# Kernel tuning notes

Measured on AMD Instinct MI355X. Metric: run time of the kernel, lower is better.

Reference implementation:

```python
import jax, jax.numpy as jnp
import numpy as np

N_NODES = 100000
N_EDGES = 1600000
GENE_DIM = 256
HID = 128
NUM_CLASSES = 2
BN_EPS = 1e-5


def setup_inputs() -> dict:
    key = jax.random.key(0)
    ks = jax.random.split(key, 24)
    g = lambda k, shape, scale: (jax.random.normal(k, shape, dtype=jnp.float32) * scale)
    inp = {
        "x": g(ks[0], (N_NODES, GENE_DIM), 1.0),
        "edge_index": jax.random.randint(ks[1], (2, N_EDGES), 0, N_NODES, dtype=jnp.int64),
        # GCNConv weights (glorot-ish scale) and biases
        "W1": g(ks[2], (GENE_DIM, HID), 1.0 / np.sqrt(GENE_DIM)), "b1": jnp.zeros((HID,), jnp.float32),
        "W2": g(ks[3], (HID, 2 * HID), 1.0 / np.sqrt(HID)), "b2": jnp.zeros((2 * HID,), jnp.float32),
        "W3": g(ks[4], (2 * HID, HID), 1.0 / np.sqrt(2 * HID)), "b3": jnp.zeros((HID,), jnp.float32),
        "W4": g(ks[5], (HID, HID // 2), 1.0 / np.sqrt(HID)), "b4": jnp.zeros((HID // 2,), jnp.float32),
        "Wc": g(ks[6], (HID // 2, NUM_CLASSES), 1.0 / np.sqrt(HID // 2)), "bc": jnp.zeros((NUM_CLASSES,), jnp.float32),
        # BatchNorm affine params
        "g1": jnp.ones((HID,), jnp.float32), "be1": jnp.zeros((HID,), jnp.float32),
        "g2": jnp.ones((2 * HID,), jnp.float32), "be2": jnp.zeros((2 * HID,), jnp.float32),
        "g3": jnp.ones((HID,), jnp.float32), "be3": jnp.zeros((HID,), jnp.float32),
        "g4": jnp.ones((HID // 2,), jnp.float32), "be4": jnp.zeros((HID // 2,), jnp.float32),
    }
    return inp


def _batchnorm(h, gamma, beta):
    # training-mode BatchNorm1d: per-feature batch stats (biased variance)
    mean = h.mean(axis=0)
    var = ((h - mean) ** 2).mean(axis=0)
    return gamma * (h - mean) * jax.lax.rsqrt(var + BN_EPS) + beta


def _gcn_conv(h, W, b, src, dst, norm, n):
    # PyG GCNConv: linear transform, then sym-normalized aggregation over
    # edges (self-loops already included in src/dst/norm), then bias.
    m = h @ W                                   # [n, d_out]
    msg = m[src] * norm[:, None]                # [E+n, d_out] gather
    agg = jax.ops.segment_sum(msg, dst, num_segments=n)  # scatter-add
    return agg + b


def reference(x, edge_index, W1, b1, W2, b2, W3, b3, W4, b4, Wc, bc,
              g1, be1, g2, be2, g3, be3, g4, be4):
    n = x.shape[0]
    loop = jnp.arange(n, dtype=edge_index.dtype)
    src = jnp.concatenate([edge_index[0], loop])  # add self-loops
    dst = jnp.concatenate([edge_index[1], loop])
    deg = jax.ops.segment_sum(jnp.ones_like(dst, dtype=x.dtype), dst, num_segments=n)
    dinv = jax.lax.rsqrt(jnp.maximum(deg, 1.0))
    norm = dinv[src] * dinv[dst]                  # D^-1/2 (A+I) D^-1/2

    h = jax.nn.relu(_gcn_conv(x, W1, b1, src, dst, norm, n))
    h = _batchnorm(h, g1, be1)
    h = jax.nn.relu(_gcn_conv(h, W2, b2, src, dst, norm, n))
    h = _batchnorm(h, g2, be2)
    h = jax.nn.relu(_gcn_conv(h, W3, b3, src, dst, norm, n))
    h = _batchnorm(h, g3, be3)
    out4 = jax.nn.relu(_gcn_conv(h, W4, b4, src, dst, norm, n))
    bn4 = _batchnorm(out4, g4, be4)
    logits = bn4 @ Wc + bc
    return (logits, out4, bn4)
```

## Files before the change

### kernel.cpp

```cpp
#include <hip/hip_runtime.h>
#include <hip/hip_bf16.h>

#define N_NODES 100000
#define N_EDGES 1600000
#define NB ((N_NODES + 255) / 256)
#define CHUNK 16384
#define NBLK ((N_EDGES + CHUNK - 1) / CHUNK)

typedef short sh8 __attribute__((ext_vector_type(8)));
typedef float f32x4 __attribute__((ext_vector_type(4)));

__device__ __forceinline__ float bf2f(unsigned short s) {
    return __uint_as_float(((unsigned int)s) << 16);
}
__device__ __forceinline__ unsigned short f2bf(float f) {
    unsigned int u = __float_as_uint(f);
    unsigned int r = (u + 0x7FFFu + ((u >> 16) & 1u)) >> 16;
    return (unsigned short)r;
}
__device__ __forceinline__ float blo(unsigned int u) { return __uint_as_float(u << 16); }
__device__ __forceinline__ float bhi(unsigned int u) { return __uint_as_float(u & 0xffff0000u); }


__global__ __launch_bounds__(256) void k_hist(const int* __restrict__ ei, int* __restrict__ histG) {
    __shared__ int hist[NB];
    int blk = blockIdx.x, t = threadIdx.x;
    for (int b = t; b < NB; b += 256) hist[b] = 0;
    __syncthreads();
    int e0 = blk * CHUNK;
    int e1 = min(e0 + CHUNK, N_EDGES);
    for (int e = e0 + t; e < e1; e += 256) atomicAdd(&hist[ei[N_EDGES + e] >> 8], 1);
    __syncthreads();
    for (int b = t; b < NB; b += 256) histG[b * NBLK + blk] = hist[b];
}

__global__ __launch_bounds__(128) void k_scanrow(int* __restrict__ histG, int* __restrict__ rowsum) {
    __shared__ int sm[128];
    int b = blockIdx.x, t = threadIdx.x;
    int v = (t < NBLK) ? histG[b * NBLK + t] : 0;
    sm[t] = v; __syncthreads();
    for (int d = 1; d < 128; d <<= 1) {
        int add = (t >= d) ? sm[t - d] : 0;
        __syncthreads(); sm[t] += add; __syncthreads();
    }
    if (t < NBLK) histG[b * NBLK + t] = sm[t] - v;
    if (t == 127) rowsum[b] = sm[127];
}

__global__ __launch_bounds__(512) void k_scanbkt(const int* __restrict__ rowsum, int* __restrict__ rowbase) {
    __shared__ int sm[512];
    int t = threadIdx.x;
    int v = (t < NB) ? rowsum[t] : 0;
    sm[t] = v; __syncthreads();
    for (int d = 1; d < 512; d <<= 1) {
        int add = (t >= d) ? sm[t - d] : 0;
        __syncthreads(); sm[t] += add; __syncthreads();
    }
    if (t <= NB) rowbase[t] = sm[t] - v;
}

__global__ __launch_bounds__(256) void k_part(const int* __restrict__ ei, const int* __restrict__ histG,
                                              const int* __restrict__ rowbase, unsigned* __restrict__ pairs) {
    __shared__ int cur[NB];
    int blk = blockIdx.x, t = threadIdx.x;
    for (int b = t; b < NB; b += 256) cur[b] = rowbase[b] + histG[b * NBLK + blk];
    __syncthreads();
    int e0 = blk * CHUNK;
    int e1 = min(e0 + CHUNK, N_EDGES);
    for (int e = e0 + t; e < e1; e += 256) {
        int s = ei[e], d = ei[N_EDGES + e];
        int pos = atomicAdd(&cur[d >> 8], 1);
        pairs[pos] = ((unsigned)s << 8) | (unsigned)(d & 255);
    }
}

__global__ __launch_bounds__(256) void k_bsort(const unsigned* __restrict__ pairs, const int* __restrict__ rowbase,
                                               int* __restrict__ col, int* __restrict__ basep,
                                               int* __restrict__ deg, float* __restrict__ dinv,
                                               float* __restrict__ sdeg) {
    __shared__ int cnt[256];
    __shared__ int sm[256];
    __shared__ int cur[256];
    int b = blockIdx.x, t = threadIdx.x;
    int base = rowbase[b], end = rowbase[b + 1];
    cnt[t] = 0; __syncthreads();
    for (int e = base + t; e < end; e += 256) atomicAdd(&cnt[pairs[e] & 255], 1);
    __syncthreads();
    int v = cnt[t];
    sm[t] = v; __syncthreads();
    for (int d = 1; d < 256; d <<= 1) {
        int add = (t >= d) ? sm[t - d] : 0;
        __syncthreads(); sm[t] += add; __syncthreads();
    }
    int excl = sm[t] - v;
    cur[t] = excl;
    int gd = (b << 8) + t;
    if (gd < N_NODES) {
        basep[gd] = base + excl;
        deg[gd] = v;
        dinv[gd] = rsqrtf((float)(v + 1));
        sdeg[gd] = sqrtf((float)(v + 1));
    }
    __syncthreads();
    for (int e = base + t; e < end; e += 256) {
        unsigned p = pairs[e];
        int pos = atomicAdd(&cur[p & 255], 1);
        col[base + pos] = (int)(p >> 8);
    }
}

__global__ __launch_bounds__(256) void k_svec(const int* __restrict__ col, const int* __restrict__ basep,
                                              const int* __restrict__ deg, const float* __restrict__ dinv,
                                              float* __restrict__ svec) {
    int w = (blockIdx.x * 256 + threadIdx.x) >> 6;
    if (w >= N_NODES) return;
    int lane = threadIdx.x & 63;
    int start = basep[w], cnt = deg[w];
    float s = 0.f;
    for (int j = lane; j < cnt; j += 64) s += dinv[col[start + j]];
#pragma unroll
    for (int off = 32; off; off >>= 1) s += __shfl_down(s, off, 64);
    if (lane == 0) { float di = dinv[w]; svec[w] = di * (s + di); }
}


__global__ void k_wconv_all(const float* __restrict__ W1, const float* __restrict__ W2,
                            const float* __restrict__ W3, const float* __restrict__ W4,
                            unsigned short* __restrict__ Wt1, unsigned short* __restrict__ Wt2,
                            unsigned short* __restrict__ Wt3, unsigned short* __restrict__ Wt4) {
    int idx = blockIdx.x * 256 + threadIdx.x;
    const float* W; unsigned short* Wt; int K, N, base;
    if (idx < 32768)       { W = W1; Wt = Wt1; K = 256; N = 128; base = 0; }
    else if (idx < 65536)  { W = W2; Wt = Wt2; K = 128; N = 256; base = 32768; }
    else if (idx < 98304)  { W = W3; Wt = Wt3; K = 256; N = 128; base = 65536; }
    else if (idx < 106496) { W = W4; Wt = Wt4; K = 128; N = 64;  base = 98304; }
    else return;
    int li = idx - base;
    int n = li / K, k = li - n * K;
    Wt[li] = f2bf(W[(size_t)k * N + n]);
}


template <int BN, int NWM, int NWN, int AMODE, bool BIASRELU, bool DSCALE, bool STATS>
__global__ __launch_bounds__(256) void k_gemm_bf(const void* __restrict__ Ain,
                                                 const unsigned short* __restrict__ Wt,
                                                 const float* __restrict__ ss,
                                                 const float* __restrict__ svec,
                                                 const float* __restrict__ bias,
                                                 const float* __restrict__ dinv,
                                                 unsigned short* __restrict__ Mout,
                                                 float* __restrict__ sums,
                                                 int K, int NTOT) {
    constexpr int BK = 64;
    constexpr int LDA = BK + 8;
    constexpr int MF = 128 / (16 * NWM);
    constexpr int NF = BN / (16 * NWN);
    __shared__ unsigned short As[128 * LDA];
    __shared__ unsigned short Bs[BN * LDA];
    const int tid = threadIdx.x;
    const int lane = tid & 63;
    const int w = tid >> 6;
    const int wm = w / NWN, wn = w % NWN;
    const int row0 = blockIdx.x * 128;
    const int col0 = blockIdx.y * BN;

    f32x4 acc[MF][NF];
#pragma unroll
    for (int i = 0; i < MF; ++i)
#pragma unroll
        for (int j = 0; j < NF; ++j)
#pragma unroll
            for (int r = 0; r < 4; ++r) acc[i][j][r] = 0.f;

    const int sr = tid >> 3;
    const int scc = (tid & 7) * 8;

    for (int k0 = 0; k0 < K; k0 += BK) {
#pragma unroll
        for (int p = 0; p < 4; ++p) {
            int r = p * 32 + sr;
            int gr = row0 + r;
            alignas(16) unsigned short tmp[8];
            if constexpr (AMODE == 0) {
                const float* Af = (const float*)Ain;
                float4 v0 = make_float4(0.f, 0.f, 0.f, 0.f), v1 = v0;
                if (gr < N_NODES) {
                    const float* p0 = Af + (size_t)gr * K + k0 + scc;
                    v0 = *(const float4*)p0;
                    v1 = *(const float4*)(p0 + 4);
                }
                tmp[0] = f2bf(v0.x); tmp[1] = f2bf(v0.y); tmp[2] = f2bf(v0.z); tmp[3] = f2bf(v0.w);
                tmp[4] = f2bf(v1.x); tmp[5] = f2bf(v1.y); tmp[6] = f2bf(v1.z); tmp[7] = f2bf(v1.w);
            } else {
                const unsigned short* Ab = (const unsigned short*)Ain;
                uint4 raw = make_uint4(0, 0, 0, 0);
                if (gr < N_NODES) raw = *(const uint4*)(Ab + (size_t)gr * K + k0 + scc);
                const unsigned short* pr = (const unsigned short*)&raw;
                float sv = 1.f;
                if constexpr (AMODE == 2) sv = (gr < N_NODES) ? svec[gr] : 0.f;
#pragma unroll
                for (int q = 0; q < 8; ++q) {
                    float sc = ss[k0 + scc + q];
                    float sh = ss[256 + k0 + scc + q];
                    float val;
                    if constexpr (AMODE == 2) val = bf2f(pr[q]) * sc + sh * sv;
                    else val = bf2f(pr[q]) * sc + sh;
                    tmp[q] = f2bf(val);
                }
            }
            *(uint4*)&As[r * LDA + scc] = *(const uint4*)tmp;
        }
        constexpr int BP = (BN * BK) / 2048;
#pragma unroll
        for (int p = 0; p < BP; ++p) {
            int r = p * 32 + sr;
            uint4 raw = *(const uint4*)(Wt + (size_t)(col0 + r) * K + k0 + scc);
            *(uint4*)&Bs[r * LDA + scc] = raw;
        }
        __syncthreads();
#pragma unroll
        for (int ks = 0; ks < 2; ++ks) {
            sh8 af[MF], bfr[NF];
#pragma unroll
            for (int i = 0; i < MF; ++i)
                af[i] = *(const sh8*)&As[(wm * MF * 16 + i * 16 + (lane & 15)) * LDA + ks * 32 + (lane >> 4) * 8];
#pragma unroll
            for (int j = 0; j < NF; ++j)
                bfr[j] = *(const sh8*)&Bs[(wn * NF * 16 + j * 16 + (lane & 15)) * LDA + ks * 32 + (lane >> 4) * 8];
#pragma unroll
            for (int i = 0; i < MF; ++i)
#pragma unroll
                for (int j = 0; j < NF; ++j)
                    acc[i][j] = __builtin_amdgcn_mfma_f32_16x16x32_bf16(af[i], bfr[j], acc[i][j], 0, 0, 0);
        }
        __syncthreads();
    }

    float cs[NF], cs2[NF];
    if constexpr (STATS) {
#pragma unroll
        for (int j = 0; j < NF; ++j) { cs[j] = 0.f; cs2[j] = 0.f; }
    }
#pragma unroll
    for (int i = 0; i < MF; ++i) {
#pragma unroll
        for (int r = 0; r < 4; ++r) {
            int grow = row0 + wm * MF * 16 + i * 16 + (lane >> 4) * 4 + r;
            if (grow >= N_NODES) continue;
            float rsc = 1.f;
            if constexpr (DSCALE) rsc = dinv[grow];
#pragma unroll
            for (int j = 0; j < NF; ++j) {
                int gcol = col0 + wn * NF * 16 + j * 16 + (lane & 15);
                float v = acc[i][j][r];
                if constexpr (BIASRELU) v = fmaxf(v + bias[gcol], 0.f);
                if constexpr (DSCALE) v *= rsc;
                if constexpr (STATS) { cs[j] += v; cs2[j] += v * v; }
                Mout[(size_t)grow * NTOT + gcol] = f2bf(v);
            }
        }
    }
    if constexpr (STATS) {
        __shared__ float red[2][BN];
        for (int i = tid; i < 2 * BN; i += 256) ((float*)red)[i] = 0.f;
        __syncthreads();
#pragma unroll
        for (int j = 0; j < NF; ++j) {
            int lc = wn * NF * 16 + j * 16 + (lane & 15);
            atomicAdd(&red[0][lc], cs[j]);
            atomicAdd(&red[1][lc], cs2[j]);
        }
        __syncthreads();
        for (int f = tid; f < BN; f += 256) {
            atomicAdd(&sums[col0 + f], red[0][f]);
            atomicAdd(&sums[256 + col0 + f], red[1][f]);
        }
    }
}


template <int D, bool PRE, bool OUTF32, bool OUTSCALE, bool STATS, bool RESCALE>
__global__ __launch_bounds__(256) void k_agg4(const unsigned short* __restrict__ m,
                                              const int* __restrict__ col,
                                              const int* __restrict__ basep,
                                              const int* __restrict__ deg,
                                              const float* __restrict__ dinv,
                                              const float* __restrict__ sdeg,
                                              const float* __restrict__ bias,
                                              void* __restrict__ out,
                                              float* __restrict__ sums) {
    constexpr int VPL = D / 64;
    const int lane = threadIdx.x & 63;
    const int wid = threadIdx.x >> 6;
    const int fo = lane * VPL;
    const unsigned short* mfo = m + fo;
    float s1r[VPL], s2r[VPL];
    if constexpr (STATS) {
#pragma unroll
        for (int k = 0; k < VPL; ++k) { s1r[k] = 0.f; s2r[k] = 0.f; }
    }

    for (int it = 0; it < 16; ++it) {
        int w = blockIdx.x * 64 + it * 4 + wid;
        if (w >= N_NODES) continue;
        float acc[VPL];
#pragma unroll
        for (int k = 0; k < VPL; ++k) acc[k] = 0.f;

        int start = basep[w], cnt = deg[w];
        int j = 0;
        for (; j + 8 <= cnt; j += 8) {
            int sx[8];
#pragma unroll
            for (int i = 0; i < 8; ++i) sx[i] = col[start + j + i];
            if constexpr (VPL == 2) {
                unsigned u[8];
#pragma unroll
                for (int i = 0; i < 8; ++i) u[i] = *(const unsigned*)(mfo + (size_t)sx[i] * D);
#pragma unroll
                for (int i = 0; i < 8; ++i) { acc[0] += blo(u[i]); acc[1] += bhi(u[i]); }
            } else {
                float v[8];
#pragma unroll
                for (int i = 0; i < 8; ++i) v[i] = bf2f(mfo[(size_t)sx[i] * D]);
#pragma unroll
                for (int i = 0; i < 8; ++i) acc[0] += v[i];
            }
        }
        for (; j < cnt; ++j) {
            int s0 = col[start + j];
            if constexpr (VPL == 2) {
                unsigned u0 = *(const unsigned*)(mfo + (size_t)s0 * D);
                acc[0] += blo(u0); acc[1] += bhi(u0);
            } else {
                acc[0] += bf2f(mfo[(size_t)s0 * D]);
            }
        }
        if constexpr (VPL == 2) {
            unsigned u0 = *(const unsigned*)(mfo + (size_t)w * D);
            acc[0] += blo(u0); acc[1] += bhi(u0);
        } else {
            acc[0] += bf2f(mfo[(size_t)w * D]);
        }

        float di = dinv[w];
        float o[VPL];
        if constexpr (PRE) {
#pragma unroll
            for (int k = 0; k < VPL; ++k) o[k] = acc[k] * di;
        } else {
#pragma unroll
            for (int k = 0; k < VPL; ++k) {
                o[k] = fmaxf(acc[k] * di + bias[fo + k], 0.f);
                if constexpr (OUTSCALE) o[k] *= di;
            }
        }
        if constexpr (STATS) {
            float rs = 1.f;
            if constexpr (RESCALE) rs = sdeg[w];
#pragma unroll
            for (int k = 0; k < VPL; ++k) { float v = o[k] * rs; s1r[k] += v; s2r[k] += v * v; }
        }

        if constexpr (OUTF32) {
            float* of = (float*)out;
#pragma unroll
            for (int k = 0; k < VPL; ++k) of[(size_t)w * D + fo + k] = o[k];
        } else {
            unsigned short* ob = (unsigned short*)out + (size_t)w * D + fo;
            if constexpr (VPL == 2) {
                unsigned int u = (unsigned)f2bf(o[0]) | ((unsigned)f2bf(o[1]) << 16);
                *(unsigned int*)ob = u;
            } else {
                ob[0] = f2bf(o[0]);
            }
        }
    }

    if constexpr (STATS) {
        __shared__ float red[2][D];
        for (int i = threadIdx.x; i < 2 * D; i += 256) ((float*)red)[i] = 0.f;
        __syncthreads();
#pragma unroll
        for (int k = 0; k < VPL; ++k) {
            atomicAdd(&red[0][fo + k], s1r[k]);
            atomicAdd(&red[1][fo + k], s2r[k]);
        }
        __syncthreads();
        for (int f = threadIdx.x; f < D; f += 256) {
            atomicAdd(&sums[f], red[0][f]);
            atomicAdd(&sums[256 + f], red[1][f]);
        }
    }
}


template <int D>
__global__ void k_bnfin(const float* __restrict__ sums, const float* __restrict__ gamma,
                        const float* __restrict__ beta, float* __restrict__ ss) {
    int f = threadIdx.x;
    float mean = sums[f] * (1.f / N_NODES);
    float var = sums[256 + f] * (1.f / N_NODES) - mean * mean;
    float inv = rsqrtf(var + 1e-5f);
    float sc = gamma[f] * inv;
    ss[f] = sc;
    ss[256 + f] = beta[f] - mean * sc;
}


__global__ __launch_bounds__(256) void k_bnlog(const float* __restrict__ out4, const float* __restrict__ ss,
                                               const float* __restrict__ Wc, const float* __restrict__ bc,
                                               float* __restrict__ bn4, float* __restrict__ logits) {
    int gw = (blockIdx.x * 256 + threadIdx.x) >> 6;
    if (gw >= N_NODES) return;
    int f = threadIdx.x & 63;
    float v = out4[(size_t)gw * 64 + f];
    float bn = v * ss[f] + ss[256 + f];
    bn4[(size_t)gw * 64 + f] = bn;
    float a0 = bn * Wc[2 * f];
    float a1 = bn * Wc[2 * f + 1];
#pragma unroll
    for (int off = 32; off; off >>= 1) {
        a0 += __shfl_down(a0, off, 64);
        a1 += __shfl_down(a1, off, 64);
    }
    if (f == 0) {
        logits[2 * gw] = a0 + bc[0];
        logits[2 * gw + 1] = a1 + bc[1];
    }
}


extern "C" void kernel_launch(void* const* d_in, const int* in_sizes, int n_in,
                              void* d_out, int out_size, void* d_ws, size_t ws_size,
                              hipStream_t stream) {
    const float* x  = (const float*)d_in[0];
    const int* ei   = (const int*)d_in[1];
    const float* W1 = (const float*)d_in[2];  const float* b1  = (const float*)d_in[3];
    const float* W2 = (const float*)d_in[4];  const float* b2  = (const float*)d_in[5];
    const float* W3 = (const float*)d_in[6];  const float* b3  = (const float*)d_in[7];
    const float* W4 = (const float*)d_in[8];  const float* b4  = (const float*)d_in[9];
    const float* Wc = (const float*)d_in[10]; const float* bc  = (const float*)d_in[11];
    const float* g1 = (const float*)d_in[12]; const float* be1 = (const float*)d_in[13];
    const float* g2 = (const float*)d_in[14]; const float* be2 = (const float*)d_in[15];
    const float* g3 = (const float*)d_in[16]; const float* be3 = (const float*)d_in[17];
    const float* g4 = (const float*)d_in[18]; const float* be4 = (const float*)d_in[19];

    char* wsb = (char*)d_ws;
    size_t off = 0;
    auto alloc = [&](size_t bytes) -> void* {
        void* p = wsb + off;
        off = (off + bytes + 511) & ~(size_t)511;
        return p;
    };
    int* deg     = (int*)alloc((size_t)N_NODES * 4);
    int* basep   = (int*)alloc((size_t)N_NODES * 4);
    float* dinv  = (float*)alloc((size_t)N_NODES * 4);
    float* sdeg  = (float*)alloc((size_t)N_NODES * 4);
    float* svec  = (float*)alloc((size_t)N_NODES * 4);
    int* col     = (int*)alloc((size_t)N_EDGES * 4);
    unsigned* pairs = (unsigned*)alloc((size_t)N_EDGES * 4);
    int* histG   = (int*)alloc((size_t)NB * NBLK * 4);
    int* rowsum  = (int*)alloc((size_t)NB * 4);
    int* rowbase = (int*)alloc((size_t)(NB + 1) * 4);
    float* sums  = (float*)alloc(2048 * 4);
    float* ss    = (float*)alloc(512 * 4);
    unsigned short* Wt1 = (unsigned short*)alloc((size_t)256 * 128 * 2);
    unsigned short* Wt2 = (unsigned short*)alloc((size_t)128 * 256 * 2);
    unsigned short* Wt3 = (unsigned short*)alloc((size_t)256 * 128 * 2);
    unsigned short* Wt4 = (unsigned short*)alloc((size_t)128 * 64 * 2);
    unsigned short* mb = (unsigned short*)alloc((size_t)N_NODES * 128 * 2);
    unsigned short* hb = (unsigned short*)alloc((size_t)N_NODES * 256 * 2);

    float* sums1 = sums, *sums2 = sums + 512, *sums3 = sums + 1024, *sums4 = sums + 1536;

    float* outLogits = (float*)d_out;
    float* out4 = outLogits + (size_t)N_NODES * 2;
    float* bn4  = out4 + (size_t)N_NODES * 64;

    hipMemsetAsync(sums, 0, 2048 * 4, stream);

    k_hist<<<NBLK, 256, 0, stream>>>(ei, histG);
    k_scanrow<<<NB, 128, 0, stream>>>(histG, rowsum);
    k_scanbkt<<<1, 512, 0, stream>>>(rowsum, rowbase);
    k_part<<<NBLK, 256, 0, stream>>>(ei, histG, rowbase, pairs);
    k_bsort<<<NB, 256, 0, stream>>>(pairs, rowbase, col, basep, deg, dinv, sdeg);
    k_svec<<<(N_NODES + 3) / 4, 256, 0, stream>>>(col, basep, deg, dinv, svec);

    k_wconv_all<<<(106496 + 255) / 256, 256, 0, stream>>>(W1, W2, W3, W4, Wt1, Wt2, Wt3, Wt4);

    const int GBM = (N_NODES + 127) / 128;
    const int AB4 = (N_NODES + 63) / 64;

    k_gemm_bf<128, 2, 2, 0, false, true, false><<<dim3(GBM, 1), 256, 0, stream>>>(
        x, Wt1, nullptr, nullptr, nullptr, dinv, mb, nullptr, 256, 128);
    k_agg4<128, false, false, true, true, true><<<AB4, 256, 0, stream>>>(
        mb, col, basep, deg, dinv, sdeg, b1, hb, sums1);
    k_bnfin<128><<<1, 128, 0, stream>>>(sums1, g1, be1, ss);

    k_agg4<128, true, false, false, false, false><<<AB4, 256, 0, stream>>>(
        hb, col, basep, deg, dinv, nullptr, nullptr, mb, nullptr);
    k_gemm_bf<128, 2, 2, 2, true, false, true><<<dim3(GBM, 2), 256, 0, stream>>>(
        mb, Wt2, ss, svec, b2, nullptr, hb, sums2, 128, 256);
    k_bnfin<256><<<1, 256, 0, stream>>>(sums2, g2, be2, ss);

    k_gemm_bf<128, 2, 2, 1, false, true, false><<<dim3(GBM, 1), 256, 0, stream>>>(
        hb, Wt3, ss, nullptr, nullptr, dinv, mb, nullptr, 256, 128);
    k_agg4<128, false, false, false, true, false><<<AB4, 256, 0, stream>>>(
        mb, col, basep, deg, dinv, nullptr, b3, hb, sums3);
    k_bnfin<128><<<1, 128, 0, stream>>>(sums3, g3, be3, ss);

    k_gemm_bf<64, 4, 1, 1, false, true, false><<<dim3(GBM, 1), 256, 0, stream>>>(
        hb, Wt4, ss, nullptr, nullptr, dinv, mb, nullptr, 128, 64);
    k_agg4<64, false, true, false, true, false><<<AB4, 256, 0, stream>>>(
        mb, col, basep, deg, dinv, nullptr, b4, out4, sums4);
    k_bnfin<64><<<1, 64, 0, stream>>>(sums4, g4, be4, ss);
    k_bnlog<<<(N_NODES * 64 + 255) / 256, 256, 0, stream>>>(out4, ss, Wc, bc, bn4, outLogits);
}
```

Measured before the change: 703.5 us.

## Fold BN finalize into consumer kernels and give each aggregation block one node per wave

Removes the four single-block k_bnfin launches by computing BatchNorm scale and shift from the raw sums inside the consuming GEMM (into shared memory) and inside k_bnlog. The aggregation kernel now processes one node per wave, with a grid of N/4 blocks instead of blocks looping over 64 nodes. This cuts launch and serialization overhead and raises parallelism in aggregation. In exchange, every block recomputes the BN coefficients and does its own shared and global atomic reduction for the statistics, which greatly increases the number of global atomics.

New measurement: 2.219 ms. +215.4%, slower.

```diff
diff --git a/kernel.cpp b/kernel.cpp
--- a/kernel.cpp
+++ b/kernel.cpp
@@ -144,12 +144,14 @@
 template <int BN, int NWM, int NWN, int AMODE, bool BIASRELU, bool DSCALE, bool STATS>
 __global__ __launch_bounds__(256) void k_gemm_bf(const void* __restrict__ Ain,
                                                  const unsigned short* __restrict__ Wt,
-                                                 const float* __restrict__ ss,
+                                                 const float* __restrict__ sums_in,
+                                                 const float* __restrict__ gamma,
+                                                 const float* __restrict__ beta,
                                                  const float* __restrict__ svec,
                                                  const float* __restrict__ bias,
                                                  const float* __restrict__ dinv,
                                                  unsigned short* __restrict__ Mout,
-                                                 float* __restrict__ sums,
+                                                 float* __restrict__ sums_out,
                                                  int K, int NTOT) {
     constexpr int BK = 64;
     constexpr int LDA = BK + 8;
@@ -157,12 +159,26 @@
     constexpr int NF = BN / (16 * NWN);
     __shared__ unsigned short As[128 * LDA];
     __shared__ unsigned short Bs[BN * LDA];
+    __shared__ float ss_sc[256];
+    __shared__ float ss_sh[256];
     const int tid = threadIdx.x;
     const int lane = tid & 63;
     const int w = tid >> 6;
     const int wm = w / NWN, wn = w % NWN;
     const int row0 = blockIdx.x * 128;
     const int col0 = blockIdx.y * BN;
+
+    if constexpr (AMODE >= 1) {
+        for (int f = tid; f < K; f += 256) {
+            float mean = sums_in[f] * (1.f / N_NODES);
+            float var = sums_in[256 + f] * (1.f / N_NODES) - mean * mean;
+            float inv = rsqrtf(var + 1e-5f);
+            float sc = gamma[f] * inv;
+            ss_sc[f] = sc;
+            ss_sh[f] = beta[f] - mean * sc;
+        }
+        __syncthreads();
+    }
 
     f32x4 acc[MF][NF];
 #pragma unroll
@@ -200,8 +216,8 @@
                 if constexpr (AMODE == 2) sv = (gr < N_NODES) ? svec[gr] : 0.f;
 #pragma unroll
                 for (int q = 0; q < 8; ++q) {
-                    float sc = ss[k0 + scc + q];
-                    float sh = ss[256 + k0 + scc + q];
+                    float sc = ss_sc[k0 + scc + q];
+                    float sh = ss_sh[k0 + scc + q];
                     float val;
                     if constexpr (AMODE == 2) val = bf2f(pr[q]) * sc + sh * sv;
                     else val = bf2f(pr[q]) * sc + sh;
@@ -272,15 +288,15 @@
         }
         __syncthreads();
         for (int f = tid; f < BN; f += 256) {
-            atomicAdd(&sums[col0 + f], red[0][f]);
-            atomicAdd(&sums[256 + col0 + f], red[1][f]);
+            atomicAdd(&sums_out[col0 + f], red[0][f]);
+            atomicAdd(&sums_out[256 + col0 + f], red[1][f]);
         }
     }
 }
 
 
 template <int D, bool PRE, bool OUTF32, bool OUTSCALE, bool STATS, bool RESCALE>
-__global__ __launch_bounds__(256) void k_agg4(const unsigned short* __restrict__ m,
+__global__ __launch_bounds__(256) void k_agg5(const unsigned short* __restrict__ m,
                                               const int* __restrict__ col,
                                               const int* __restrict__ basep,
                                               const int* __restrict__ deg,
@@ -294,15 +310,20 @@
     const int wid = threadIdx.x >> 6;
     const int fo = lane * VPL;
     const unsigned short* mfo = m + fo;
-    float s1r[VPL], s2r[VPL];
-    if constexpr (STATS) {
-#pragma unroll
-        for (int k = 0; k < VPL; ++k) { s1r[k] = 0.f; s2r[k] = 0.f; }
-    }
-
-    for (int it = 0; it < 16; ++it) {
-        int w = blockIdx.x * 64 + it * 4 + wid;
-        if (w >= N_NODES) continue;
+    const int w = blockIdx.x * 4 + wid;
+    const bool valid = (w < N_NODES);
+
+    float bvals[VPL];
+    if constexpr (!PRE) {
+#pragma unroll
+        for (int k = 0; k < VPL; ++k) bvals[k] = bias[fo + k];
+    }
+
+    float o[VPL];
+#pragma unroll
+    for (int k = 0; k < VPL; ++k) o[k] = 0.f;
+
+    if (valid) {
         float acc[VPL];
 #pragma unroll
         for (int k = 0; k < VPL; ++k) acc[k] = 0.f;
@@ -344,22 +365,15 @@
         }
 
         float di = dinv[w];
-        float o[VPL];
         if constexpr (PRE) {
 #pragma unroll
             for (int k = 0; k < VPL; ++k) o[k] = acc[k] * di;
         } else {
 #pragma unroll
             for (int k = 0; k < VPL; ++k) {
-                o[k] = fmaxf(acc[k] * di + bias[fo + k], 0.f);
+                o[k] = fmaxf(acc[k] * di + bvals[k], 0.f);
                 if constexpr (OUTSCALE) o[k] *= di;
             }
-        }
-        if constexpr (STATS) {
-            float rs = 1.f;
-            if constexpr (RESCALE) rs = sdeg[w];
-#pragma unroll
-            for (int k = 0; k < VPL; ++k) { float v = o[k] * rs; s1r[k] += v; s2r[k] += v * v; }
         }
 
         if constexpr (OUTF32) {
@@ -381,10 +395,13 @@
         __shared__ float red[2][D];
         for (int i = threadIdx.x; i < 2 * D; i += 256) ((float*)red)[i] = 0.f;
         __syncthreads();
+        float rs = 1.f;
+        if constexpr (RESCALE) rs = valid ? sdeg[w] : 0.f;
 #pragma unroll
         for (int k = 0; k < VPL; ++k) {
-            atomicAdd(&red[0][fo + k], s1r[k]);
-            atomicAdd(&red[1][fo + k], s2r[k]);
+            float v = o[k] * rs;
+            atomicAdd(&red[0][fo + k], v);
+            atomicAdd(&red[1][fo + k], v * v);
         }
         __syncthreads();
         for (int f = threadIdx.x; f < D; f += 256) {
@@ -395,27 +412,20 @@
 }
 
 
-template <int D>
-__global__ void k_bnfin(const float* __restrict__ sums, const float* __restrict__ gamma,
-                        const float* __restrict__ beta, float* __restrict__ ss) {
-    int f = threadIdx.x;
-    float mean = sums[f] * (1.f / N_NODES);
-    float var = sums[256 + f] * (1.f / N_NODES) - mean * mean;
-    float inv = rsqrtf(var + 1e-5f);
-    float sc = gamma[f] * inv;
-    ss[f] = sc;
-    ss[256 + f] = beta[f] - mean * sc;
-}
-
-
-__global__ __launch_bounds__(256) void k_bnlog(const float* __restrict__ out4, const float* __restrict__ ss,
+__global__ __launch_bounds__(256) void k_bnlog(const float* __restrict__ out4, const float* __restrict__ sums,
+                                               const float* __restrict__ gamma, const float* __restrict__ beta,
                                                const float* __restrict__ Wc, const float* __restrict__ bc,
                                                float* __restrict__ bn4, float* __restrict__ logits) {
     int gw = (blockIdx.x * 256 + threadIdx.x) >> 6;
     if (gw >= N_NODES) return;
     int f = threadIdx.x & 63;
+    float mean = sums[f] * (1.f / N_NODES);
+    float var = sums[256 + f] * (1.f / N_NODES) - mean * mean;
+    float inv = rsqrtf(var + 1e-5f);
+    float sc = gamma[f] * inv;
+    float sh = beta[f] - mean * sc;
     float v = out4[(size_t)gw * 64 + f];
-    float bn = v * ss[f] + ss[256 + f];
+    float bn = v * sc + sh;
     bn4[(size_t)gw * 64 + f] = bn;
     float a0 = bn * Wc[2 * f];
     float a1 = bn * Wc[2 * f + 1];
@@ -464,7 +474,6 @@
     int* rowsum  = (int*)alloc((size_t)NB * 4);
     int* rowbase = (int*)alloc((size_t)(NB + 1) * 4);
     float* sums  = (float*)alloc(2048 * 4);
-    float* ss    = (float*)alloc(512 * 4);
     unsigned short* Wt1 = (unsigned short*)alloc((size_t)256 * 128 * 2);
     unsigned short* Wt2 = (unsigned short*)alloc((size_t)128 * 256 * 2);
     unsigned short* Wt3 = (unsigned short*)alloc((size_t)256 * 128 * 2);
@@ -490,30 +499,26 @@
     k_wconv_all<<<(106496 + 255) / 256, 256, 0, stream>>>(W1, W2, W3, W4, Wt1, Wt2, Wt3, Wt4);
 
     const int GBM = (N_NODES + 127) / 128;
-    const int AB4 = (N_NODES + 63) / 64;
+    const int AB = (N_NODES + 3) / 4;
 
     k_gemm_bf<128, 2, 2, 0, false, true, false><<<dim3(GBM, 1), 256, 0, stream>>>(
-        x, Wt1, nullptr, nullptr, nullptr, dinv, mb, nullptr, 256, 128);
-    k_agg4<128, false, false, true, true, true><<<AB4, 256, 0, stream>>>(
+        x, Wt1, nullptr, nullptr, nullptr, nullptr, nullptr, dinv, mb, nullptr, 256, 128);
+    k_agg5<128, false, false, true, true, true><<<AB, 256, 0, stream>>>(
         mb, col, basep, deg, dinv, sdeg, b1, hb, sums1);
-    k_bnfin<128><<<1, 128, 0, stream>>>(sums1, g1, be1, ss);
-
-    k_agg4<128, true, false, false, false, false><<<AB4, 256, 0, stream>>>(
+
+    k_agg5<128, true, false, false, false, false><<<AB, 256, 0, stream>>>(
         hb, col, basep, deg, dinv, nullptr, nullptr, mb, nullptr);
     k_gemm_bf<128, 2, 2, 2, true, false, true><<<dim3(GBM, 2), 256, 0, stream>>>(
-        mb, Wt2, ss, svec, b2, nullptr, hb, sums2, 128, 256);
-    k_bnfin<256><<<1, 256, 0, stream>>>(sums2, g2, be2, ss);
+        mb, Wt2, sums1, g1, be1, svec, b2, nullptr, hb, sums2, 128, 256);
 
     k_gemm_bf<128, 2, 2, 1, false, true, false><<<dim3(GBM, 1), 256, 0, stream>>>(
-        hb, Wt3, ss, nullptr, nullptr, dinv, mb, nullptr, 256, 128);
-    k_agg4<128, false, false, false, true, false><<<AB4, 256, 0, stream>>>(
+        hb, Wt3, sums2, g2, be2, nullptr, nullptr, dinv, mb, nullptr, 256, 128);
+    k_agg5<128, false, false, false, true, false><<<AB, 256, 0, stream>>>(
         mb, col, basep, deg, dinv, nullptr, b3, hb, sums3);
-    k_bnfin<128><<<1, 128, 0, stream>>>(sums3, g3, be3, ss);
 
     k_gemm_bf<64, 4, 1, 1, false, true, false><<<dim3(GBM, 1), 256, 0, stream>>>(
-        hb, Wt4, ss, nullptr, nullptr, dinv, mb, nullptr, 128, 64);
-    k_agg4<64, false, true, false, true, false><<<AB4, 256, 0, stream>>>(
+        hb, Wt4, sums3, g3, be3, nullptr, nullptr, dinv, mb, nullptr, 128, 64);
+    k_agg5<64, false, true, false, true, false><<<AB, 256, 0, stream>>>(
         mb, col, basep, deg, dinv, nullptr, b4, out4, sums4);
-    k_bnfin<64><<<1, 64, 0, stream>>>(sums4, g4, be4, ss);
-    k_bnlog<<<(N_NODES * 64 + 255) / 256, 256, 0, stream>>>(out4, ss, Wc, bc, bn4, outLogits);
-}
+    k_bnlog<<<(N_NODES * 64 + 255) / 256, 256, 0, stream>>>(out4, sums4, g4, be4, Wc, bc, bn4, outLogits);
+}
```
